# Performance work log

Measured on AMD Instinct MI355X. Metric: run time of the kernel, lower is better.

Reference implementation:

```python
import jax, jax.numpy as jnp
import numpy as np

HEADS = 8
DIM_HEAD = 64
BN_EPS = 1e-5

def setup_inputs() -> dict:
    key = jax.random.key(0)
    ks = jax.random.split(key, 6)
    B, N, D = 8, 1024, 512
    inner = HEADS * DIM_HEAD  # 512
    return {
        "x": jax.random.normal(ks[0], (B, N, D), dtype=jnp.float32),
        "w_qkv": jax.random.normal(ks[1], (D, 3 * inner), dtype=jnp.float32) * (D ** -0.5),
        "conv_w": jax.random.normal(ks[2], (HEADS, HEADS), dtype=jnp.float32) * (HEADS ** -0.5),
        "conv_b": jax.random.normal(ks[3], (HEADS,), dtype=jnp.float32) * 0.02,
        "bn_gamma": jnp.ones((HEADS,), dtype=jnp.float32),
        "bn_beta": jnp.zeros((HEADS,), dtype=jnp.float32),
        "w_out": jax.random.normal(ks[4], (inner, D), dtype=jnp.float32) * (inner ** -0.5),
        "b_out": jnp.zeros((D,), dtype=jnp.float32),
    }

def reference(x, w_qkv, conv_w, conv_b, bn_gamma, bn_beta, w_out, b_out):
    B, N, D = x.shape
    H, dh = HEADS, DIM_HEAD
    scale = dh ** -0.5
    qkv = x @ w_qkv  # [B, N, 3*H*dh]
    q, k, v = jnp.split(qkv, 3, axis=-1)
    # b n (h d) -> b h n d
    q = q.reshape(B, N, H, dh).transpose(0, 2, 1, 3)
    k = k.reshape(B, N, H, dh).transpose(0, 2, 1, 3)
    v = v.reshape(B, N, H, dh).transpose(0, 2, 1, 3)
    attn = jnp.einsum('bhnd,bhmd->bhnm', q, k) * scale
    attn = jax.nn.softmax(attn, axis=-1)
    # 1x1 conv across heads (channels = heads)
    attn = jnp.einsum('gh,bhnm->bgnm', conv_w, attn) + conv_b[None, :, None, None]
    # BatchNorm2d in training mode: batch stats over (B, N, N) per head, biased variance
    mean = attn.mean(axis=(0, 2, 3), keepdims=True)
    var = attn.var(axis=(0, 2, 3), keepdims=True)
    attn = (attn - mean) * jax.lax.rsqrt(var + BN_EPS)
    attn = attn * bn_gamma[None, :, None, None] + bn_beta[None, :, None, None]
    # reatten_scale = 1.0 (transform_scale=False)
    out = jnp.einsum('bhnm,bhmd->bhnd', attn, v)
    out = out.transpose(0, 2, 1, 3).reshape(B, N, H * dh)  # b h n d -> b n (h d)
    return out @ w_out + b_out
```

## Files before the change

kernel.cpp:

```cpp
#include <hip/hip_runtime.h>
#include <math.h>


#define Bz 8
#define Nn 1024
#define Dd 512
#define Hh 8
#define DH 64
#define INNER 512
#define QW 1536
#define SCALE 0.125f
#define BN_EPS 1e-5f

typedef short bf16x8 __attribute__((ext_vector_type(8)));
typedef float f32x4 __attribute__((ext_vector_type(4)));

#define MFMA(a, b, c) __builtin_amdgcn_mfma_f32_16x16x32_bf16((a), (b), (c), 0, 0, 0)

__device__ __forceinline__ unsigned short f2b(float f) {
  union { float f; unsigned u; } v; v.f = f;
  unsigned r = v.u + 0x7fffu + ((v.u >> 16) & 1u);
  return (unsigned short)(r >> 16);
}
__device__ __forceinline__ float b2f(unsigned short s) {
  union { unsigned u; float f; } v; v.u = ((unsigned)s) << 16;
  return v.f;
}

#define WB_QKV 0u
#define WB_VT (WB_QKV + 25165824u)
#define WB_WQT (WB_VT + 8388608u)
#define WB_WOT (WB_WQT + 1572864u)
#define WB_O1 (WB_WOT + 524288u)
#define WB_SG (WB_O1 + 16777216u)
#define WB_RINV (WB_SG + 134217728u)
#define WB_VSUM (WB_RINV + 262144u)
#define WB_STATS (WB_VSUM + 16384u)
#define WB_AC (WB_STATS + 64u)

__global__ __launch_bounds__(256) void k_transpose(const float* __restrict__ src,
                                                   unsigned short* __restrict__ dst,
                                                   int R, int C) {
  __shared__ float tile[32][33];
  const int tc = blockIdx.x * 32, tr = blockIdx.y * 32;
  const int lx = threadIdx.x & 31, ly = threadIdx.x >> 5;
#pragma unroll
  for (int i = 0; i < 32; i += 8)
    tile[ly + i][lx] = src[(size_t)(tr + ly + i) * C + tc + lx];
  __syncthreads();
#pragma unroll
  for (int i = 0; i < 32; i += 8)
    dst[(size_t)(tc + ly + i) * R + tr + lx] = f2b(tile[lx][ly + i]);
}

__global__ __launch_bounds__(256) void k_qkv(const float* __restrict__ X,
                                             const unsigned short* __restrict__ WQT,
                                             unsigned short* __restrict__ qkv,
                                             unsigned short* __restrict__ vT) {
  extern __shared__ char smem[];
  unsigned short(*sA)[40] = (unsigned short(*)[40])smem;
  unsigned short(*sB)[40] = (unsigned short(*)[40])(smem + 128 * 40 * 2);
  unsigned short* sEp = (unsigned short*)smem;
  const int t = threadIdx.x;
  const int col0 = blockIdx.x * 128;
  const int row0 = blockIdx.y * 128;
  const bool isqk = (col0 < 2 * INNER);
  const int l = t & 63, w = t >> 6;
  const int wm = (w & 1) * 64, wn = (w >> 1) * 64;
  const int lm = l & 15, lq = l >> 4;
  const int srow = t >> 1, skc = (t & 1) * 16;
  f32x4 acc[4][4] = {};
  for (int k0 = 0; k0 < Dd; k0 += 32) {
    {
      const float* src = X + (size_t)(row0 + srow) * Dd + k0 + skc;
      unsigned short tmp[16];
#pragma unroll
      for (int c4 = 0; c4 < 4; c4++) {
        float4 f = *(const float4*)(src + c4 * 4);
        tmp[c4 * 4 + 0] = f2b(f.x);
        tmp[c4 * 4 + 1] = f2b(f.y);
        tmp[c4 * 4 + 2] = f2b(f.z);
        tmp[c4 * 4 + 3] = f2b(f.w);
      }
      *(uint4*)&sA[srow][skc] = *(uint4*)tmp;
      *(uint4*)&sA[srow][skc + 8] = *(uint4*)(tmp + 8);
    }
    {
      const unsigned short* srcB = WQT + (size_t)(col0 + srow) * Dd + k0 + skc;
      *(uint4*)&sB[srow][skc] = *(const uint4*)srcB;
      *(uint4*)&sB[srow][skc + 8] = *(const uint4*)(srcB + 8);
    }
    __syncthreads();
    bf16x8 af[4], bfr[4];
#pragma unroll
    for (int i = 0; i < 4; i++) af[i] = *(const bf16x8*)&sA[wm + 16 * i + lm][lq * 8];
#pragma unroll
    for (int j = 0; j < 4; j++) bfr[j] = *(const bf16x8*)&sB[wn + 16 * j + lm][lq * 8];
    if (isqk) {
#pragma unroll
      for (int i = 0; i < 4; i++)
#pragma unroll
        for (int j = 0; j < 4; j++) acc[i][j] = MFMA(bfr[i], af[j], acc[i][j]);
    } else {
#pragma unroll
      for (int i = 0; i < 4; i++)
#pragma unroll
        for (int j = 0; j < 4; j++) acc[i][j] = MFMA(af[i], bfr[j], acc[i][j]);
    }
    __syncthreads();
  }
  if (isqk) {
#pragma unroll
    for (int jc = 0; jc < 4; jc++)
#pragma unroll
      for (int ir = 0; ir < 4; ir++) {
        unsigned short us[4];
#pragma unroll
        for (int r = 0; r < 4; r++) us[r] = f2b(acc[jc][ir][r]);
        *(uint2*)&sEp[(wm + 16 * ir + lm) * 136 + wn + 16 * jc + 4 * lq] = *(uint2*)us;
      }
    __syncthreads();
    const int row = t >> 1, half = t & 1;
    const unsigned short* src = &sEp[row * 136 + half * 64];
    unsigned short* dst = qkv + (size_t)(row0 + row) * QW + col0 + half * 64;
#pragma unroll
    for (int c = 0; c < 8; c++) *(uint4*)(dst + c * 8) = *(const uint4*)(src + c * 8);
  } else {
#pragma unroll
    for (int ir = 0; ir < 4; ir++)
#pragma unroll
      for (int jc = 0; jc < 4; jc++) {
        unsigned short us[4];
#pragma unroll
        for (int r = 0; r < 4; r++) us[r] = f2b(acc[ir][jc][r]);
        *(uint2*)&sEp[(wn + 16 * jc + lm) * 136 + wm + 16 * ir + 4 * lq] = *(uint2*)us;
      }
    __syncthreads();
    const int row = t >> 1, half = t & 1;
    const int gd = col0 - 2 * INNER + row;
    const int bq = row0 >> 10, mseq0 = row0 & 1023;
    const unsigned short* src = &sEp[row * 136 + half * 64];
    unsigned short* dst =
        vT + (((size_t)(bq * Hh + (gd >> 6)) * DH + (gd & 63)) << 10) + mseq0 + half * 64;
#pragma unroll
    for (int c = 0; c < 8; c++) *(uint4*)(dst + c * 8) = *(const uint4*)(src + c * 8);
  }
}

__global__ __launch_bounds__(256) void k_vsum(const unsigned short* __restrict__ vT,
                                              float* __restrict__ vsum) {
  const int bg = blockIdx.x;
  const int d = threadIdx.x >> 2, qq = threadIdx.x & 3;
  __shared__ float red[64][4];
  const unsigned short* p = vT + ((size_t)bg * DH + d) * Nn + qq * 256;
  float s = 0.f;
  for (int m = 0; m < 256; m += 4) {
    uint2 rr = *(const uint2*)(p + m);
    s += b2f((unsigned short)(rr.x & 0xffff)) + b2f((unsigned short)(rr.x >> 16)) +
         b2f((unsigned short)(rr.y & 0xffff)) + b2f((unsigned short)(rr.y >> 16));
  }
  red[d][qq] = s;
  __syncthreads();
  if (threadIdx.x < 64)
    vsum[(size_t)bg * DH + threadIdx.x] =
        red[threadIdx.x][0] + red[threadIdx.x][1] + red[threadIdx.x][2] + red[threadIdx.x][3];
}

__global__ __launch_bounds__(512, 4) void k_sgen(const unsigned short* __restrict__ qkv,
                                                 unsigned short* __restrict__ Sg,
                                                 float* __restrict__ rinvG) {
  __shared__ unsigned short sK[64 * 80];
  __shared__ unsigned short sSout[128 * 72];
  const int b = blockIdx.x, ntile = blockIdx.y, h = blockIdx.z;
  const int n0 = ntile * 128;
  const int t = threadIdx.x;
  const int w = t >> 6, l = t & 63;
  const int lm = l & 15, lq = l >> 4;
  bf16x8 qf[2];
  {
    const unsigned short* qp =
        qkv + (size_t)(b * Nn + n0 + w * 16 + lm) * QW + h * DH + lq * 8;
    qf[0] = *(const bf16x8*)(qp);
    qf[1] = *(const bf16x8*)(qp + 32);
  }
  float psum = 0.f;
  for (int m0 = 0; m0 < Nn; m0 += 64) {
    {
      const int row = t >> 3, c = (t & 7) * 8;
      *(uint4*)&sK[row * 80 + c] =
          *(const uint4*)(qkv + (size_t)(b * Nn + m0 + row) * QW + INNER + h * DH + c);
    }
    __syncthreads();
    f32x4 lac[4] = {};
#pragma unroll
    for (int j = 0; j < 4; j++) {
      bf16x8 a0 = *(const bf16x8*)&sK[(16 * j + lm) * 80 + lq * 8];
      bf16x8 a1 = *(const bf16x8*)&sK[(16 * j + lm) * 80 + 32 + lq * 8];
      lac[j] = MFMA(a0, qf[0], lac[j]);
      lac[j] = MFMA(a1, qf[1], lac[j]);
    }
#pragma unroll
    for (int j = 0; j < 4; j++) {
      unsigned short us[4];
#pragma unroll
      for (int r = 0; r < 4; r++) {
        float e = __expf(lac[j][r] * SCALE);
        psum += e;
        us[r] = f2b(e);
      }
      *(uint2*)&sSout[(w * 16 + lm) * 72 + 16 * j + 4 * lq] = *(uint2*)us;
    }
    __syncthreads();
    {
      const int row = t >> 2, c = (t & 3) * 16;
      const unsigned short* src = &sSout[row * 72 + c];
      unsigned short* dst =
          Sg + ((size_t)(b * Hh + h) << 20) + (size_t)(n0 + row) * Nn + m0 + c;
      *(uint4*)dst = *(const uint4*)src;
      *(uint4*)(dst + 8) = *(const uint4*)(src + 8);
    }
  }
  psum += __shfl_xor(psum, 16);
  psum += __shfl_xor(psum, 32);
  if (lq == 0) rinvG[(size_t)(b * Hh + h) * Nn + n0 + w * 16 + lm] = 1.0f / psum;
}

__global__ __launch_bounds__(512, 4) void k_mixsv(const unsigned short* __restrict__ Sg,
                                                  const unsigned short* __restrict__ vT,
                                                  const float* __restrict__ rinvG,
                                                  const float* __restrict__ conv_w,
                                                  float* __restrict__ O1,
                                                  float* __restrict__ stats) {
  __shared__ unsigned short sU[8 * 16 * 72];
  __shared__ float sRed[8][16];
  const int b = blockIdx.x;
  const int n0 = blockIdx.y * 16;
  const int t = threadIdx.x;
  const int w = t >> 6, l = t & 63;
  const int lm = l & 15, lq = l >> 4;
  const int mxn = t >> 5, mxm = (t & 31) * 2;
  float cw[64];
#pragma unroll
  for (int i = 0; i < 64; i++) cw[i] = conv_w[i];
  float rv[8];
#pragma unroll
  for (int h = 0; h < 8; h++) rv[h] = rinvG[(size_t)(b * Hh + h) * Nn + n0 + mxn];
  f32x4 oacc[4] = {};
  float su[8] = {}, su2[8] = {};
  for (int m0 = 0; m0 < Nn; m0 += 64) {
    {
      float sx[8], sy[8];
#pragma unroll
      for (int h = 0; h < 8; h++) {
        unsigned pk = *(const unsigned*)(Sg + ((size_t)(b * Hh + h) << 20) +
                                         (size_t)(n0 + mxn) * Nn + m0 + mxm);
        sx[h] = b2f((unsigned short)(pk & 0xffff)) * rv[h];
        sy[h] = b2f((unsigned short)(pk >> 16)) * rv[h];
      }
#pragma unroll
      for (int g = 0; g < 8; g++) {
        float u0 = 0.f, u1 = 0.f;
#pragma unroll
        for (int h = 0; h < 8; h++) {
          u0 += cw[g * 8 + h] * sx[h];
          u1 += cw[g * 8 + h] * sy[h];
        }
        su[g] += u0 + u1;
        su2[g] += u0 * u0 + u1 * u1;
        *(unsigned*)&sU[(g * 16 + mxn) * 72 + mxm] =
            (unsigned)f2b(u0) | ((unsigned)f2b(u1) << 16);
      }
    }
    __syncthreads();
    {
      bf16x8 uf0 = *(const bf16x8*)&sU[(w * 16 + lm) * 72 + lq * 8];
      bf16x8 uf1 = *(const bf16x8*)&sU[(w * 16 + lm) * 72 + 32 + lq * 8];
#pragma unroll
      for (int j = 0; j < 4; j++) {
        const unsigned short* vp =
            vT + (((size_t)(b * Hh + w) * DH + 16 * j + lm) << 10) + m0 + lq * 8;
        bf16x8 v0 = *(const bf16x8*)vp;
        bf16x8 v1 = *(const bf16x8*)(vp + 32);
        oacc[j] = MFMA(uf0, v0, oacc[j]);
        oacc[j] = MFMA(uf1, v1, oacc[j]);
      }
    }
    __syncthreads();
  }
#pragma unroll
  for (int j = 0; j < 4; j++)
#pragma unroll
    for (int r = 0; r < 4; r++)
      O1[((size_t)(b * Hh + w) * Nn + n0 + lq * 4 + r) * DH + 16 * j + lm] = oacc[j][r];
#pragma unroll
  for (int g = 0; g < 8; g++) {
    float a = su[g], q = su2[g];
    for (int off = 32; off; off >>= 1) {
      a += __shfl_down(a, off);
      q += __shfl_down(q, off);
    }
    if (l == 0) {
      sRed[w][g] = a;
      sRed[w][8 + g] = q;
    }
  }
  __syncthreads();
  if (t < 16) {
    float s = 0.f;
#pragma unroll
    for (int ww = 0; ww < 8; ww++) s += sRed[ww][t];
    atomicAdd(&stats[t], s);
  }
}

__global__ void k_alpha(const float* __restrict__ stats, const float* __restrict__ bn_gamma,
                        const float* __restrict__ bn_beta, float* __restrict__ ac) {
  const int g = threadIdx.x;
  if (g < 8) {
    const float cnt = (float)Bz * (float)Nn * (float)Nn;
    float Eu = stats[g] / cnt;
    float Eu2 = stats[8 + g] / cnt;
    float inv = rsqrtf(Eu2 - Eu * Eu + BN_EPS);
    float alpha = bn_gamma[g] * inv;
    ac[g] = alpha;
    ac[8 + g] = bn_beta[g] - Eu * alpha;
  }
}

__global__ __launch_bounds__(256) void k_out(const float* __restrict__ O1,
                                             const float* __restrict__ vsum,
                                             const float* __restrict__ ac,
                                             const unsigned short* __restrict__ WOT,
                                             const float* __restrict__ bout,
                                             float* __restrict__ out) {
  __shared__ unsigned short sA[128][40];
  __shared__ unsigned short sB[128][40];
  __shared__ float sAl[16];
  const int t = threadIdx.x;
  if (t < 16) sAl[t] = ac[t];
  const int col0 = blockIdx.x * 128, row0 = blockIdx.y * 128;
  const int l = t & 63, w = t >> 6;
  const int wm = (w & 1) * 64, wn = (w >> 1) * 64;
  const int lm = l & 15, lq = l >> 4;
  const int srow = t >> 1, skc = (t & 1) * 16;
  const int b = row0 >> 10;
  const int nn = (row0 + srow) & 1023;
  f32x4 acc[4][4] = {};
  __syncthreads();
  for (int k0 = 0; k0 < INNER; k0 += 32) {
    {
      const int k = k0 + skc;
      const int g = k >> 6, dd = k & 63;
      const float al = sAl[g], cc = sAl[8 + g];
      const float* op = O1 + ((size_t)(b * Hh + g) * Nn + nn) * DH + dd;
      const float* vp = vsum + (size_t)(b * Hh + g) * DH + dd;
      unsigned short tmp[16];
#pragma unroll
      for (int c4 = 0; c4 < 4; c4++) {
        float4 o4 = *(const float4*)(op + c4 * 4);
        float4 v4 = *(const float4*)(vp + c4 * 4);
        tmp[c4 * 4 + 0] = f2b(al * o4.x + cc * v4.x);
        tmp[c4 * 4 + 1] = f2b(al * o4.y + cc * v4.y);
        tmp[c4 * 4 + 2] = f2b(al * o4.z + cc * v4.z);
        tmp[c4 * 4 + 3] = f2b(al * o4.w + cc * v4.w);
      }
      *(uint4*)&sA[srow][skc] = *(uint4*)tmp;
      *(uint4*)&sA[srow][skc + 8] = *(uint4*)(tmp + 8);
    }
    {
      const unsigned short* srcB = WOT + (size_t)(col0 + srow) * INNER + k0 + skc;
      *(uint4*)&sB[srow][skc] = *(const uint4*)srcB;
      *(uint4*)&sB[srow][skc + 8] = *(const uint4*)(srcB + 8);
    }
    __syncthreads();
    bf16x8 af[4], bfr[4];
#pragma unroll
    for (int i = 0; i < 4; i++) af[i] = *(const bf16x8*)&sA[wm + 16 * i + lm][lq * 8];
#pragma unroll
    for (int j = 0; j < 4; j++) bfr[j] = *(const bf16x8*)&sB[wn + 16 * j + lm][lq * 8];
#pragma unroll
    for (int i = 0; i < 4; i++)
#pragma unroll
      for (int j = 0; j < 4; j++) acc[i][j] = MFMA(af[i], bfr[j], acc[i][j]);
    __syncthreads();
  }
#pragma unroll
  for (int j = 0; j < 4; j++) {
    const int col = col0 + wn + 16 * j + lm;
    const float bo = bout[col];
#pragma unroll
    for (int i = 0; i < 4; i++) {
      const int rbase = row0 + wm + 16 * i + lq * 4;
#pragma unroll
      for (int r = 0; r < 4; r++) out[(size_t)(rbase + r) * Dd + col] = acc[i][j][r] + bo;
    }
  }
}

extern "C" void kernel_launch(void* const* d_in, const int* in_sizes, int n_in,
                              void* d_out, int out_size, void* d_ws, size_t ws_size,
                              hipStream_t stream) {
  const float* x = (const float*)d_in[0];
  const float* w_qkv = (const float*)d_in[1];
  const float* conv_w = (const float*)d_in[2];
  const float* bn_gamma = (const float*)d_in[4];
  const float* bn_beta = (const float*)d_in[5];
  const float* w_out = (const float*)d_in[6];
  const float* b_out = (const float*)d_in[7];
  char* ws = (char*)d_ws;
  unsigned short* QKV = (unsigned short*)(ws + WB_QKV);
  unsigned short* VT = (unsigned short*)(ws + WB_VT);
  unsigned short* WQT = (unsigned short*)(ws + WB_WQT);
  unsigned short* WOT = (unsigned short*)(ws + WB_WOT);
  float* O1 = (float*)(ws + WB_O1);
  unsigned short* SG = (unsigned short*)(ws + WB_SG);
  float* RINV = (float*)(ws + WB_RINV);
  float* VSUM = (float*)(ws + WB_VSUM);
  float* STATS = (float*)(ws + WB_STATS);
  float* AC = (float*)(ws + WB_AC);

  hipMemsetAsync(STATS, 0, 64, stream);
  k_transpose<<<dim3(48, 16), 256, 0, stream>>>(w_qkv, WQT, 512, 1536);
  k_transpose<<<dim3(16, 16), 256, 0, stream>>>(w_out, WOT, 512, 512);
  k_qkv<<<dim3(12, 64), 256, 34816, stream>>>(x, WQT, QKV, VT);
  k_vsum<<<64, 256, 0, stream>>>(VT, VSUM);
  k_sgen<<<dim3(8, 8, 8), 512, 0, stream>>>(QKV, SG, RINV);
  k_mixsv<<<dim3(8, 64), 512, 0, stream>>>(SG, VT, RINV, conv_w, O1, STATS);
  k_alpha<<<1, 64, 0, stream>>>(STATS, bn_gamma, bn_beta, AC);
  k_out<<<dim3(4, 64), 256, 0, stream>>>(O1, VSUM, AC, WOT, b_out, (float*)d_out);
}
```

Measured before the change: 277.3 us.

## Interleave heads in score buffer, split key range across blocks, pre-convert activations

The score buffer is now stored head-interleaved ([b,n,m,h]), so the head-mixing kernel reads all 8 heads of a score with one contiguous load. Score generation processes all heads per block over half the key range and accumulates row sums with atomics. The mix/SV kernel is split over two key halves writing separate partial outputs, register-prefetches scores and drops a barrier. x is converted to bf16 once up front, and the BN affine plus partial-sum merge is moved to a separate elementwise kernel producing bf16 input for the output GEMM. This adds extra launches and workspace traffic, and the dropped barrier depends on the double-buffered shared tile being safe to reuse.

```diff
diff --git a/kernel.cpp b/kernel.cpp
--- a/kernel.cpp
+++ b/kernel.cpp
@@ -27,16 +27,29 @@
   return v.f;
 }
 
-#define WB_QKV 0u
-#define WB_VT (WB_QKV + 25165824u)
-#define WB_WQT (WB_VT + 8388608u)
-#define WB_WOT (WB_WQT + 1572864u)
-#define WB_O1 (WB_WOT + 524288u)
-#define WB_SG (WB_O1 + 16777216u)
-#define WB_RINV (WB_SG + 134217728u)
-#define WB_VSUM (WB_RINV + 262144u)
-#define WB_STATS (WB_VSUM + 16384u)
-#define WB_AC (WB_STATS + 64u)
+#define WB_XB 0u
+#define WB_QKV 8388608u
+#define WB_O1A 0u
+#define WB_O1B 16777216u
+#define WB_VT 33554432u
+#define WB_SG 41943040u
+#define WB_O1BF WB_SG
+#define WB_WQT 176160768u
+#define WB_WOT 177733632u
+#define WB_RSUM 178257920u
+#define WB_VSUM 178520064u
+#define WB_STATS 178536448u
+#define WB_AC 178536512u
+
+__global__ __launch_bounds__(256) void k_xbf(const float* __restrict__ X,
+                                             unsigned short* __restrict__ XB) {
+  const size_t i = ((size_t)blockIdx.x * 256 + threadIdx.x) * 8;
+  float4 f0 = *(const float4*)(X + i);
+  float4 f1 = *(const float4*)(X + i + 4);
+  unsigned short o[8] = {f2b(f0.x), f2b(f0.y), f2b(f0.z), f2b(f0.w),
+                         f2b(f1.x), f2b(f1.y), f2b(f1.z), f2b(f1.w)};
+  *(uint4*)(XB + i) = *(uint4*)o;
+}
 
 __global__ __launch_bounds__(256) void k_transpose(const float* __restrict__ src,
                                                    unsigned short* __restrict__ dst,
@@ -53,7 +66,7 @@
     dst[(size_t)(tc + ly + i) * R + tr + lx] = f2b(tile[lx][ly + i]);
 }
 
-__global__ __launch_bounds__(256) void k_qkv(const float* __restrict__ X,
+__global__ __launch_bounds__(256) void k_qkv(const unsigned short* __restrict__ XB,
                                              const unsigned short* __restrict__ WQT,
                                              unsigned short* __restrict__ qkv,
                                              unsigned short* __restrict__ vT) {
@@ -72,18 +85,9 @@
   f32x4 acc[4][4] = {};
   for (int k0 = 0; k0 < Dd; k0 += 32) {
     {
-      const float* src = X + (size_t)(row0 + srow) * Dd + k0 + skc;
-      unsigned short tmp[16];
-#pragma unroll
-      for (int c4 = 0; c4 < 4; c4++) {
-        float4 f = *(const float4*)(src + c4 * 4);
-        tmp[c4 * 4 + 0] = f2b(f.x);
-        tmp[c4 * 4 + 1] = f2b(f.y);
-        tmp[c4 * 4 + 2] = f2b(f.z);
-        tmp[c4 * 4 + 3] = f2b(f.w);
-      }
-      *(uint4*)&sA[srow][skc] = *(uint4*)tmp;
-      *(uint4*)&sA[srow][skc + 8] = *(uint4*)(tmp + 8);
+      const unsigned short* src = XB + (size_t)(row0 + srow) * Dd + k0 + skc;
+      *(uint4*)&sA[srow][skc] = *(const uint4*)src;
+      *(uint4*)&sA[srow][skc + 8] = *(const uint4*)(src + 8);
     }
     {
       const unsigned short* srcB = WQT + (size_t)(col0 + srow) * Dd + k0 + skc;
@@ -168,73 +172,91 @@
 
 __global__ __launch_bounds__(512, 4) void k_sgen(const unsigned short* __restrict__ qkv,
                                                  unsigned short* __restrict__ Sg,
-                                                 float* __restrict__ rinvG) {
-  __shared__ unsigned short sK[64 * 80];
-  __shared__ unsigned short sSout[128 * 72];
-  const int b = blockIdx.x, ntile = blockIdx.y, h = blockIdx.z;
-  const int n0 = ntile * 128;
+                                                 float* __restrict__ rsum) {
+  __shared__ unsigned short sK[8 * 32 * 72];
+  __shared__ unsigned short sT[32 * 264];
+  const int b = blockIdx.x;
+  const int n0 = blockIdx.y * 32;
+  const int mh = blockIdx.z;
   const int t = threadIdx.x;
   const int w = t >> 6, l = t & 63;
   const int lm = l & 15, lq = l >> 4;
-  bf16x8 qf[2];
-  {
+  bf16x8 qf[2][2];
+#pragma unroll
+  for (int i = 0; i < 2; i++) {
     const unsigned short* qp =
-        qkv + (size_t)(b * Nn + n0 + w * 16 + lm) * QW + h * DH + lq * 8;
-    qf[0] = *(const bf16x8*)(qp);
-    qf[1] = *(const bf16x8*)(qp + 32);
-  }
-  float psum = 0.f;
-  for (int m0 = 0; m0 < Nn; m0 += 64) {
-    {
-      const int row = t >> 3, c = (t & 7) * 8;
-      *(uint4*)&sK[row * 80 + c] =
-          *(const uint4*)(qkv + (size_t)(b * Nn + m0 + row) * QW + INNER + h * DH + c);
-    }
-    __syncthreads();
-    f32x4 lac[4] = {};
-#pragma unroll
-    for (int j = 0; j < 4; j++) {
-      bf16x8 a0 = *(const bf16x8*)&sK[(16 * j + lm) * 80 + lq * 8];
-      bf16x8 a1 = *(const bf16x8*)&sK[(16 * j + lm) * 80 + 32 + lq * 8];
-      lac[j] = MFMA(a0, qf[0], lac[j]);
-      lac[j] = MFMA(a1, qf[1], lac[j]);
-    }
-#pragma unroll
-    for (int j = 0; j < 4; j++) {
-      unsigned short us[4];
-#pragma unroll
-      for (int r = 0; r < 4; r++) {
-        float e = __expf(lac[j][r] * SCALE);
-        psum += e;
-        us[r] = f2b(e);
-      }
-      *(uint2*)&sSout[(w * 16 + lm) * 72 + 16 * j + 4 * lq] = *(uint2*)us;
-    }
-    __syncthreads();
-    {
-      const int row = t >> 2, c = (t & 3) * 16;
-      const unsigned short* src = &sSout[row * 72 + c];
+        qkv + (size_t)(b * Nn + n0 + 16 * i + lm) * QW + w * DH + lq * 8;
+    qf[i][0] = *(const bf16x8*)qp;
+    qf[i][1] = *(const bf16x8*)(qp + 32);
+  }
+  float psum[2] = {0.f, 0.f};
+  for (int it = 0; it < 16; it++) {
+    const int m0 = mh * 512 + it * 32;
+    {
+#pragma unroll
+      for (int s = 0; s < 4; s++) {
+        const int c = t + s * 512;
+        const int hh = c >> 8, mm = (c >> 3) & 31, qq = c & 7;
+        *(uint4*)&sK[(hh * 32 + mm) * 72 + qq * 8] = *(const uint4*)(
+            qkv + (size_t)(b * Nn + m0 + mm) * QW + INNER + hh * DH + qq * 8);
+      }
+    }
+    __syncthreads();
+    f32x4 lac[2][2] = {};
+#pragma unroll
+    for (int jm = 0; jm < 2; jm++) {
+      bf16x8 ka0 = *(const bf16x8*)&sK[(w * 32 + 16 * jm + lm) * 72 + lq * 8];
+      bf16x8 ka1 = *(const bf16x8*)&sK[(w * 32 + 16 * jm + lm) * 72 + 32 + lq * 8];
+#pragma unroll
+      for (int i = 0; i < 2; i++) {
+        lac[i][jm] = MFMA(ka0, qf[i][0], lac[i][jm]);
+        lac[i][jm] = MFMA(ka1, qf[i][1], lac[i][jm]);
+      }
+    }
+#pragma unroll
+    for (int i = 0; i < 2; i++)
+#pragma unroll
+      for (int jm = 0; jm < 2; jm++)
+#pragma unroll
+        for (int r = 0; r < 4; r++) {
+          float e = __expf(lac[i][jm][r] * SCALE);
+          psum[i] += e;
+          sT[(16 * i + lm) * 264 + (16 * jm + 4 * lq + r) * 8 + w] = f2b(e);
+        }
+    __syncthreads();
+    {
+      const int row = t >> 4, ck = t & 15;
       unsigned short* dst =
-          Sg + ((size_t)(b * Hh + h) << 20) + (size_t)(n0 + row) * Nn + m0 + c;
+          Sg + (((size_t)(b * Nn + n0 + row) << 10) + m0) * 8 + ck * 16;
+      const unsigned short* src = &sT[row * 264 + ck * 16];
       *(uint4*)dst = *(const uint4*)src;
       *(uint4*)(dst + 8) = *(const uint4*)(src + 8);
     }
   }
-  psum += __shfl_xor(psum, 16);
-  psum += __shfl_xor(psum, 32);
-  if (lq == 0) rinvG[(size_t)(b * Hh + h) * Nn + n0 + w * 16 + lm] = 1.0f / psum;
+#pragma unroll
+  for (int i = 0; i < 2; i++) {
+    psum[i] += __shfl_xor(psum[i], 16);
+    psum[i] += __shfl_xor(psum[i], 32);
+  }
+  if (lq == 0) {
+    atomicAdd(&rsum[(size_t)(b * Hh + w) * Nn + n0 + lm], psum[0]);
+    atomicAdd(&rsum[(size_t)(b * Hh + w) * Nn + n0 + 16 + lm], psum[1]);
+  }
 }
 
 __global__ __launch_bounds__(512, 4) void k_mixsv(const unsigned short* __restrict__ Sg,
                                                   const unsigned short* __restrict__ vT,
-                                                  const float* __restrict__ rinvG,
+                                                  const float* __restrict__ rsum,
                                                   const float* __restrict__ conv_w,
-                                                  float* __restrict__ O1,
+                                                  float* __restrict__ O1A,
+                                                  float* __restrict__ O1B,
                                                   float* __restrict__ stats) {
-  __shared__ unsigned short sU[8 * 16 * 72];
+  __shared__ unsigned short sU[2][8][16][68];
   __shared__ float sRed[8][16];
   const int b = blockIdx.x;
   const int n0 = blockIdx.y * 16;
+  const int mbase = blockIdx.z * 512;
+  float* __restrict__ O1 = blockIdx.z ? O1B : O1A;
   const int t = threadIdx.x;
   const int w = t >> 6, l = t & 63;
   const int lm = l & 15, lq = l >> 4;
@@ -244,18 +266,34 @@
   for (int i = 0; i < 64; i++) cw[i] = conv_w[i];
   float rv[8];
 #pragma unroll
-  for (int h = 0; h < 8; h++) rv[h] = rinvG[(size_t)(b * Hh + h) * Nn + n0 + mxn];
+  for (int h = 0; h < 8; h++) rv[h] = 1.0f / rsum[(size_t)(b * Hh + h) * Nn + n0 + mxn];
+  const unsigned short* sN = Sg + ((size_t)(b * Nn + n0 + mxn) << 13);
   f32x4 oacc[4] = {};
   float su[8] = {}, su2[8] = {};
-  for (int m0 = 0; m0 < Nn; m0 += 64) {
+  uint4 sreg[2][2];
+  {
+    const unsigned short* p = sN + ((size_t)(mbase + mxm) << 3);
+    sreg[0][0] = *(const uint4*)p;
+    sreg[0][1] = *(const uint4*)(p + 8);
+  }
+#pragma unroll
+  for (int it = 0; it < 8; it++) {
+    const int cur = it & 1, nxt = cur ^ 1;
+    if (it < 7) {
+      const unsigned short* p = sN + ((size_t)(mbase + (it + 1) * 64 + mxm) << 3);
+      sreg[nxt][0] = *(const uint4*)p;
+      sreg[nxt][1] = *(const uint4*)(p + 8);
+    }
     {
       float sx[8], sy[8];
-#pragma unroll
-      for (int h = 0; h < 8; h++) {
-        unsigned pk = *(const unsigned*)(Sg + ((size_t)(b * Hh + h) << 20) +
-                                         (size_t)(n0 + mxn) * Nn + m0 + mxm);
-        sx[h] = b2f((unsigned short)(pk & 0xffff)) * rv[h];
-        sy[h] = b2f((unsigned short)(pk >> 16)) * rv[h];
+      const unsigned* pe = (const unsigned*)&sreg[cur][0];
+      const unsigned* po = (const unsigned*)&sreg[cur][1];
+#pragma unroll
+      for (int h = 0; h < 4; h++) {
+        sx[2 * h] = b2f((unsigned short)(pe[h] & 0xffff)) * rv[2 * h];
+        sx[2 * h + 1] = b2f((unsigned short)(pe[h] >> 16)) * rv[2 * h + 1];
+        sy[2 * h] = b2f((unsigned short)(po[h] & 0xffff)) * rv[2 * h];
+        sy[2 * h + 1] = b2f((unsigned short)(po[h] >> 16)) * rv[2 * h + 1];
       }
 #pragma unroll
       for (int g = 0; g < 8; g++) {
@@ -267,25 +305,23 @@
         }
         su[g] += u0 + u1;
         su2[g] += u0 * u0 + u1 * u1;
-        *(unsigned*)&sU[(g * 16 + mxn) * 72 + mxm] =
-            (unsigned)f2b(u0) | ((unsigned)f2b(u1) << 16);
-      }
-    }
-    __syncthreads();
-    {
-      bf16x8 uf0 = *(const bf16x8*)&sU[(w * 16 + lm) * 72 + lq * 8];
-      bf16x8 uf1 = *(const bf16x8*)&sU[(w * 16 + lm) * 72 + 32 + lq * 8];
+        *(unsigned*)&sU[cur][g][mxn][mxm] = (unsigned)f2b(u0) | ((unsigned)f2b(u1) << 16);
+      }
+    }
+    __syncthreads();
+    {
+      bf16x8 uf0 = *(const bf16x8*)&sU[cur][w][lm][lq * 8];
+      bf16x8 uf1 = *(const bf16x8*)&sU[cur][w][lm][32 + lq * 8];
 #pragma unroll
       for (int j = 0; j < 4; j++) {
         const unsigned short* vp =
-            vT + (((size_t)(b * Hh + w) * DH + 16 * j + lm) << 10) + m0 + lq * 8;
+            vT + (((size_t)(b * Hh + w) * DH + 16 * j + lm) << 10) + mbase + it * 64 + lq * 8;
         bf16x8 v0 = *(const bf16x8*)vp;
         bf16x8 v1 = *(const bf16x8*)(vp + 32);
         oacc[j] = MFMA(uf0, v0, oacc[j]);
         oacc[j] = MFMA(uf1, v1, oacc[j]);
       }
     }
-    __syncthreads();
   }
 #pragma unroll
   for (int j = 0; j < 4; j++)
@@ -327,17 +363,31 @@
   }
 }
 
-__global__ __launch_bounds__(256) void k_out(const float* __restrict__ O1,
-                                             const float* __restrict__ vsum,
-                                             const float* __restrict__ ac,
+__global__ __launch_bounds__(256) void k_o1aff(const float* __restrict__ O1A,
+                                               const float* __restrict__ O1B,
+                                               const float* __restrict__ vsum,
+                                               const float* __restrict__ ac,
+                                               unsigned short* __restrict__ O1BF) {
+  const size_t i4 = ((size_t)blockIdx.x * 256 + threadIdx.x) * 4;
+  const int bg = (int)(i4 >> 16);
+  const int g = bg & 7;
+  const int d = (int)(i4 & 63);
+  float4 a = *(const float4*)(O1A + i4);
+  float4 bb = *(const float4*)(O1B + i4);
+  float4 v = *(const float4*)(vsum + (size_t)bg * DH + d);
+  const float al = ac[g], cc = ac[8 + g];
+  unsigned short o[4] = {f2b(al * (a.x + bb.x) + cc * v.x), f2b(al * (a.y + bb.y) + cc * v.y),
+                         f2b(al * (a.z + bb.z) + cc * v.z), f2b(al * (a.w + bb.w) + cc * v.w)};
+  *(uint2*)(O1BF + i4) = *(uint2*)o;
+}
+
+__global__ __launch_bounds__(256) void k_out(const unsigned short* __restrict__ O1BF,
                                              const unsigned short* __restrict__ WOT,
                                              const float* __restrict__ bout,
                                              float* __restrict__ out) {
   __shared__ unsigned short sA[128][40];
   __shared__ unsigned short sB[128][40];
-  __shared__ float sAl[16];
   const int t = threadIdx.x;
-  if (t < 16) sAl[t] = ac[t];
   const int col0 = blockIdx.x * 128, row0 = blockIdx.y * 128;
   const int l = t & 63, w = t >> 6;
   const int wm = (w & 1) * 64, wn = (w >> 1) * 64;
@@ -346,26 +396,13 @@
   const int b = row0 >> 10;
   const int nn = (row0 + srow) & 1023;
   f32x4 acc[4][4] = {};
-  __syncthreads();
   for (int k0 = 0; k0 < INNER; k0 += 32) {
     {
       const int k = k0 + skc;
       const int g = k >> 6, dd = k & 63;
-      const float al = sAl[g], cc = sAl[8 + g];
-      const float* op = O1 + ((size_t)(b * Hh + g) * Nn + nn) * DH + dd;
-      const float* vp = vsum + (size_t)(b * Hh + g) * DH + dd;
-      unsigned short tmp[16];
-#pragma unroll
-      for (int c4 = 0; c4 < 4; c4++) {
-        float4 o4 = *(const float4*)(op + c4 * 4);
-        float4 v4 = *(const float4*)(vp + c4 * 4);
-        tmp[c4 * 4 + 0] = f2b(al * o4.x + cc * v4.x);
-        tmp[c4 * 4 + 1] = f2b(al * o4.y + cc * v4.y);
-        tmp[c4 * 4 + 2] = f2b(al * o4.z + cc * v4.z);
-        tmp[c4 * 4 + 3] = f2b(al * o4.w + cc * v4.w);
-      }
-      *(uint4*)&sA[srow][skc] = *(uint4*)tmp;
-      *(uint4*)&sA[srow][skc + 8] = *(uint4*)(tmp + 8);
+      const unsigned short* src = O1BF + ((size_t)(b * Hh + g) * Nn + nn) * DH + dd;
+      *(uint4*)&sA[srow][skc] = *(const uint4*)src;
+      *(uint4*)&sA[srow][skc + 8] = *(const uint4*)(src + 8);
     }
     {
       const unsigned short* srcB = WOT + (size_t)(col0 + srow) * INNER + k0 + skc;
@@ -408,24 +445,30 @@
   const float* w_out = (const float*)d_in[6];
   const float* b_out = (const float*)d_in[7];
   char* ws = (char*)d_ws;
+  unsigned short* XB = (unsigned short*)(ws + WB_XB);
   unsigned short* QKV = (unsigned short*)(ws + WB_QKV);
   unsigned short* VT = (unsigned short*)(ws + WB_VT);
+  unsigned short* SG = (unsigned short*)(ws + WB_SG);
   unsigned short* WQT = (unsigned short*)(ws + WB_WQT);
   unsigned short* WOT = (unsigned short*)(ws + WB_WOT);
-  float* O1 = (float*)(ws + WB_O1);
-  unsigned short* SG = (unsigned short*)(ws + WB_SG);
-  float* RINV = (float*)(ws + WB_RINV);
+  float* O1Ap = (float*)(ws + WB_O1A);
+  float* O1Bp = (float*)(ws + WB_O1B);
+  unsigned short* O1BF = (unsigned short*)(ws + WB_O1BF);
+  float* RSUM = (float*)(ws + WB_RSUM);
   float* VSUM = (float*)(ws + WB_VSUM);
   float* STATS = (float*)(ws + WB_STATS);
   float* AC = (float*)(ws + WB_AC);
 
   hipMemsetAsync(STATS, 0, 64, stream);
+  hipMemsetAsync(RSUM, 0, 262144, stream);
+  k_xbf<<<2048, 256, 0, stream>>>(x, XB);
   k_transpose<<<dim3(48, 16), 256, 0, stream>>>(w_qkv, WQT, 512, 1536);
   k_transpose<<<dim3(16, 16), 256, 0, stream>>>(w_out, WOT, 512, 512);
-  k_qkv<<<dim3(12, 64), 256, 34816, stream>>>(x, WQT, QKV, VT);
+  k_qkv<<<dim3(12, 64), 256, 34816, stream>>>(XB, WQT, QKV, VT);
   k_vsum<<<64, 256, 0, stream>>>(VT, VSUM);
-  k_sgen<<<dim3(8, 8, 8), 512, 0, stream>>>(QKV, SG, RINV);
-  k_mixsv<<<dim3(8, 64), 512, 0, stream>>>(SG, VT, RINV, conv_w, O1, STATS);
+  k_sgen<<<dim3(8, 32, 2), 512, 0, stream>>>(QKV, SG, RSUM);
+  k_mixsv<<<dim3(8, 64, 2), 512, 0, stream>>>(SG, VT, RSUM, conv_w, O1Ap, O1Bp, STATS);
   k_alpha<<<1, 64, 0, stream>>>(STATS, bn_gamma, bn_beta, AC);
-  k_out<<<dim3(4, 64), 256, 0, stream>>>(O1, VSUM, AC, WOT, b_out, (float*)d_out);
-}
+  k_o1aff<<<4096, 256, 0, stream>>>(O1Ap, O1Bp, VSUM, AC, O1BF);
+  k_out<<<dim3(4, 64), 256, 0, stream>>>(O1BF, WOT, b_out, (float*)d_out);
+}
```

After: 328.4 us. +18.4%, slower.
